# Kernel optimization log

Hardware: AMD Instinct MI355X
Metric: run time of the kernel (lower is better)

The kernel has to match this reference:

```python
import jax, jax.numpy as jnp
import numpy as np
import math

R, C, B, E, H, F = 64, 256, 1, 768, 12, 3072
D = E // H  # head dim = 64
EPS = 1e-6  # flax LayerNorm default


def _ln(x, s, b):
    mu = jnp.mean(x, axis=-1, keepdims=True)
    var = jnp.mean((x - mu) ** 2, axis=-1, keepdims=True)
    return (x - mu) * jax.lax.rsqrt(var + EPS) * s + b


def setup_inputs() -> dict:
    key = jax.random.key(0)
    ks = jax.random.split(key, 16)
    w = lambda k, sh: jax.random.normal(k, sh, jnp.float32) * 0.02
    z = lambda sh: jnp.zeros(sh, jnp.float32)
    return {
        "x": jax.random.normal(ks[0], (R, C, B, E), jnp.float32),
        "ln1_s": jnp.ones((E,), jnp.float32), "ln1_b": z((E,)),
        "r_wq": w(ks[1], (E, E)), "r_bq": z((E,)),
        "r_wk": w(ks[2], (E, E)), "r_bk": z((E,)),
        "r_wv": w(ks[3], (E, E)), "r_bv": z((E,)),
        "r_wo": w(ks[4], (E, E)), "r_bo": z((E,)),
        "ln2_s": jnp.ones((E,), jnp.float32), "ln2_b": z((E,)),
        "c_wq": w(ks[5], (E, E)), "c_bq": z((E,)),
        "c_wk": w(ks[6], (E, E)), "c_bk": z((E,)),
        "c_wv": w(ks[7], (E, E)), "c_bv": z((E,)),
        "c_wo": w(ks[8], (E, E)), "c_bo": z((E,)),
        "ln3_s": jnp.ones((E,), jnp.float32), "ln3_b": z((E,)),
        "f_w1": w(ks[9], (E, F)), "f_b1": z((F,)),
        "f_w2": w(ks[10], (F, E)), "f_b2": z((E,)),
    }


def reference(x, ln1_s, ln1_b, r_wq, r_bq, r_wk, r_bk, r_wv, r_bv, r_wo, r_bo,
              ln2_s, ln2_b, c_wq, c_bq, c_wk, c_bk, c_wv, c_bv, c_wo, c_bo,
              ln3_s, ln3_b, f_w1, f_b1, f_w2, f_b2):
    qkv = (R, C, B, H, D)
    # --- tied row self-attention (NOTE: original code has no residual adds) ---
    h = _ln(x, ln1_s, ln1_b)
    q = (h @ r_wq + r_bq).reshape(qkv) * (D ** -0.5 / math.sqrt(R))  # tied-row scaling
    k = (h @ r_wk + r_bk).reshape(qkv)
    v = (h @ r_wv + r_bv).reshape(qkv)
    aw = jnp.einsum('rinhd,rjnhd->hnij', q, k)  # single softmax tied across rows
    ap = jax.nn.softmax(aw, axis=-1)
    ctx = jnp.einsum('hnij,rjnhd->rinhd', ap, v).reshape(R, C, B, E)
    x = ctx @ r_wo + r_bo
    # --- column self-attention (per-column attention over rows) ---
    h = _ln(x, ln2_s, ln2_b)
    q = (h @ c_wq + c_bq).reshape(qkv) * (D ** -0.5)
    k = (h @ c_wk + c_bk).reshape(qkv)
    v = (h @ c_wv + c_bv).reshape(qkv)
    aw = jnp.einsum('icnhd,jcnhd->hcnij', q, k)
    ap = jax.nn.softmax(aw, axis=-1)
    ctx = jnp.einsum('hcnij,jcnhd->icnhd', ap, v).reshape(R, C, B, E)
    x = ctx @ c_wo + c_bo
    # --- FFN (gelu approximate=True matches flax default) ---
    h = _ln(x, ln3_s, ln3_b)
    return jax.nn.gelu(h @ f_w1 + f_b1) @ f_w2 + f_b2
```

## Files before the change

kernel.cpp:

```cpp
#include <hip/hip_runtime.h>
#include <hip/hip_bf16.h>
#include <stdint.h>
#include <stddef.h>

#define R_ 64
#define C_ 256
#define E_ 768
#define H_ 12
#define F_ 3072
#define D_ 64
#define NT_ (R_*C_)
#define HCRD_ ((size_t)H_*C_*R_*D_)

typedef float f32x4 __attribute__((ext_vector_type(4)));
typedef __bf16 bf16x8 __attribute__((ext_vector_type(8)));
typedef unsigned short us4 __attribute__((ext_vector_type(4)));
typedef unsigned short us8 __attribute__((ext_vector_type(8)));

typedef __attribute__((address_space(3))) uint32_t lds_u32;
typedef __attribute__((address_space(1))) uint32_t glb_u32;

__device__ __forceinline__ void gld16(const uint16_t* g, uint16_t* l) {
  __builtin_amdgcn_global_load_lds((const glb_u32*)g, (lds_u32*)l, 16, 0, 0);
}

__device__ __forceinline__ uint16_t f2b(float f) {
  __bf16 h = (__bf16)f;
  return *(uint16_t*)&h;
}

#define TILE_SYNC { asm volatile("s_waitcnt vmcnt(0)" ::: "memory"); \
                    __builtin_amdgcn_s_barrier(); \
                    __builtin_amdgcn_sched_barrier(0); }
#define BAR_ONLY  { __builtin_amdgcn_s_barrier(); __builtin_amdgcn_sched_barrier(0); }

enum { EP_F32B = 0, EP_GELU = 1, EP_AW = 2, EP_CTX = 3, EP_QKVROW = 4, EP_QKVCOL = 5 };

template<int EP, bool PERM>
__global__ __launch_bounds__(512, 2)
void gemm256(const uint16_t* __restrict__ A, const uint16_t* __restrict__ B,
             const float* __restrict__ bias, const float* __restrict__ biasK,
             const float* __restrict__ biasV, void* __restrict__ out,
             int N, int K, int lda, int ldb, float scale)
{
  __shared__ uint16_t As2[2][16384];
  __shared__ uint16_t Bs2[2][16384];
  const int tid  = threadIdx.x;
  const int wave = tid >> 6, lane = tid & 63;
  const int wm = wave >> 2, wn = wave & 3;
  const int lr = lane & 15, lq = lane >> 4;

  const int lin = blockIdx.x + gridDim.x * blockIdx.y;
  const int xcd = lin & 7, idx = lin >> 3;
  const int nbyx = gridDim.y >> 3;
  const int by = xcd * nbyx + idx / gridDim.x;
  const int bx = idx % gridDim.x;
  const long bm = (long)by * 256, bn = (long)bx * 256;

  const int r0 = tid >> 3;
  const int c8 = (((tid & 7) ^ (r0 & 7)) << 3);
  const uint16_t* aSrc[4];
  const uint16_t* bSrc[4];
#pragma unroll
  for (int i = 0; i < 4; ++i) {
    long am = bm + r0 + 64 * i;
    if constexpr (PERM) am = ((am & 63) << 8) | (am >> 6);
    aSrc[i] = A + am * (long)lda + c8;
    bSrc[i] = B + (bn + r0 + 64 * i) * (long)ldb + c8;
  }

  auto stage = [&](int u) {
    const int b = u & 1;
    const int kb = u << 6;
#pragma unroll
    for (int i = 0; i < 4; ++i) gld16(aSrc[i] + kb, &As2[b][tid * 8 + 4096 * i]);
#pragma unroll
    for (int i = 0; i < 4; ++i) gld16(bSrc[i] + kb, &Bs2[b][tid * 8 + 4096 * i]);
  };
  auto rdoff = [&](int row, int c) { return row * 64 + (((c ^ (row & 7))) << 3); };

  f32x4 acc[8][4];
#pragma unroll
  for (int i = 0; i < 8; ++i)
#pragma unroll
    for (int j = 0; j < 4; ++j) acc[i][j] = (f32x4){0.f, 0.f, 0.f, 0.f};

  const int nt = K >> 6;
  stage(0);
  TILE_SYNC;

  for (int t = 0; t < nt; ++t) {
    const int b = t & 1;
    if (t + 1 < nt) stage(t + 1);
#pragma unroll
    for (int kh = 0; kh < 2; ++kh) {
      const int c = kh * 4 + lq;
      bf16x8 bfr[4], afr[8];
#pragma unroll
      for (int i = 0; i < 4; ++i) bfr[i] = *(const bf16x8*)&Bs2[b][rdoff(wn * 64 + i * 16 + lr, c)];
#pragma unroll
      for (int i = 0; i < 8; ++i) afr[i] = *(const bf16x8*)&As2[b][rdoff(wm * 128 + i * 16 + lr, c)];
#pragma unroll
      for (int mi = 0; mi < 8; ++mi)
#pragma unroll
        for (int ni = 0; ni < 4; ++ni)
          acc[mi][ni] = __builtin_amdgcn_mfma_f32_16x16x32_bf16(afr[mi], bfr[ni], acc[mi][ni], 0, 0, 0);
    }
    if (t + 1 < nt) { TILE_SYNC; } else { BAR_ONLY; }
  }
  __syncthreads();

  if constexpr (EP == EP_F32B) {
#pragma unroll
    for (int mi = 0; mi < 8; ++mi)
#pragma unroll
      for (int ni = 0; ni < 4; ++ni)
#pragma unroll
        for (int r = 0; r < 4; ++r) {
          const long row = bm + wm * 128 + mi * 16 + lq * 4 + r;
          const long col = bn + wn * 64 + ni * 16 + lr;
          ((float*)out)[row * N + col] = acc[mi][ni][r] + bias[col];
        }
  } else {
    uint16_t* slabW = (wave < 4) ? &As2[0][wave * 8192] : &Bs2[0][(wave - 4) * 8192];
    const long colb = bn + wn * 64;
    int grp = 0; long cc0 = colb;
    const float* bb = bias;
    if constexpr (EP != EP_GELU) {
      grp = colb >= 1536 ? 2 : (colb >= 768 ? 1 : 0);
      cc0 = colb - (long)grp * 768;
      bb = grp == 0 ? bias : (grp == 1 ? biasK : biasV);
    }
    const bool tr = (EP != EP_GELU) && (grp == 2);
#pragma unroll
    for (int sub = 0; sub < 2; ++sub) {
      uint16_t* slab = slabW + sub * 4096;
      const long m0 = bm + wm * 128 + sub * 64;
#pragma unroll
      for (int mi = 0; mi < 4; ++mi)
#pragma unroll
        for (int ni = 0; ni < 4; ++ni)
#pragma unroll
          for (int r = 0; r < 4; ++r) {
            const int lrow = mi * 16 + lq * 4 + r;
            const int lcol = ni * 16 + lr;
            float val;
            if constexpr (EP == EP_GELU) {
              const float t = acc[sub * 4 + mi][ni][r] + bias[colb + lcol];
              const float u = 0.7978845608028654f * (t + 0.044715f * t * t * t);
              const float e = __expf(2.f * u);
              val = 0.5f * t * (2.f - 2.f / (e + 1.f));
            } else {
              val = acc[sub * 4 + mi][ni][r] + bb[cc0 + lcol];
              if (grp == 0) val *= scale;
            }
            const int sr = tr ? lcol : lrow;
            const int sc = tr ? lrow : lcol;
            const int psc = (sc & 7) | ((((sc >> 3) ^ (sr & 7))) << 3);
            slab[sr * 64 + psc] = f2b(val);
          }
      uint16_t* o16 = (uint16_t*)out;
      long obase, rstride;
      if constexpr (EP == EP_GELU) {
        obase = m0 * (long)N + colb; rstride = N;
      } else {
        const long h = cc0 >> 6;
        if constexpr (EP == EP_QKVROW) {
          const long rr = m0 >> 8, c0 = m0 & 255;
          if (grp < 2) { obase = (size_t)grp * HCRD_ + ((h * C_ + c0) * R_ + rr) * D_; rstride = R_ * D_; }
          else         { obase = 2 * HCRD_ + ((h * R_ + rr) * D_) * C_ + c0;           rstride = C_; }
        } else {
          const long cq = m0 >> 6;
          if (grp < 2) { obase = (size_t)grp * HCRD_ + ((h * C_ + cq) * R_) * D_; rstride = D_; }
          else         { obase = 2 * HCRD_ + ((h * C_ + cq) * D_) * R_;           rstride = R_; }
        }
      }
      const int rl = lane >> 3, chn = lane & 7;
#pragma unroll
      for (int pp = 0; pp < 8; ++pp) {
        const int srow = pp * 8 + rl;
        const int pch = chn ^ (srow & 7);
        us8 wv = *(const us8*)&slab[srow * 64 + pch * 8];
        *(us8*)(o16 + obase + (long)srow * rstride + chn * 8) = wv;
      }
    }
  }
}

template<int EP>
__global__ __launch_bounds__(256)
void gemm_bt(const uint16_t* __restrict__ A, const uint16_t* __restrict__ B,
             void* __restrict__ out,
             int M, int N, int K, int lda, int ldb, long sAz, long sBz)
{
  __shared__ uint16_t As[2][4096];
  __shared__ uint16_t Bs[2][4096];
  const int tid  = threadIdx.x;
  const int wave = tid >> 6, lane = tid & 63;
  const int z = blockIdx.z;

  const long bm = (long)blockIdx.y * 128;
  int kc = 0; long bnb = blockIdx.x;
  if constexpr (EP == EP_AW) { kc = blockIdx.x & 3; bnb = blockIdx.x >> 2; }
  const long bn = bnb * 128;
  const int wr = (wave >> 1) * 64;
  const int wc = (wave & 1) * 64;
  const int lr = lane & 15;
  const int lq = lane >> 4;

  const int t0 = tid, t1 = tid + 256;
  const int ar0 = t0 >> 2, ar1 = t1 >> 2;
  const int ac0 = (((t0 & 3) ^ ((ar0 >> 1) & 3)) * 8);
  const int ac1 = (((t1 & 3) ^ ((ar1 >> 1) & 3)) * 8);

  const uint16_t* a0p = A + (long)z * sAz + (bm + ar0) * (long)lda + (long)kc * 1024;
  const uint16_t* a1p = A + (long)z * sAz + (bm + ar1) * (long)lda + (long)kc * 1024;
  const uint16_t* b0p = B + (long)z * sBz + (bn + ar0) * (long)ldb + (long)kc * 1024;
  const uint16_t* b1p = B + (long)z * sBz + (bn + ar1) * (long)ldb + (long)kc * 1024;

  auto STAGE = [&](int bi, int kt) {
    gld16(a0p + kt + ac0, &As[bi][t0 * 8]);
    gld16(a1p + kt + ac1, &As[bi][t1 * 8]);
    gld16(b0p + kt + ac0, &Bs[bi][t0 * 8]);
    gld16(b1p + kt + ac1, &Bs[bi][t1 * 8]);
  };

  int apos[4], bpos[4];
#pragma unroll
  for (int i = 0; i < 4; ++i) {
    const int ra = wr + i * 16 + lr;
    const int rb = wc + i * 16 + lr;
    apos[i] = ra * 32 + (lq ^ ((ra >> 1) & 3)) * 8;
    bpos[i] = rb * 32 + (lq ^ ((rb >> 1) & 3)) * 8;
  }

  f32x4 acc[4][4];
#pragma unroll
  for (int i = 0; i < 4; ++i)
#pragma unroll
    for (int j = 0; j < 4; ++j) acc[i][j] = (f32x4){0.f, 0.f, 0.f, 0.f};

  const int nt = K >> 5;
  STAGE(0, 0);
  TILE_SYNC;

  for (int t = 0; t < nt; ++t) {
    const int b = t & 1;
    if (t + 1 < nt) STAGE(b ^ 1, (t + 1) << 5);
    bf16x8 af[4], bfm[4];
#pragma unroll
    for (int i = 0; i < 4; ++i) {
      af[i]  = *(const bf16x8*)&As[b][apos[i]];
      bfm[i] = *(const bf16x8*)&Bs[b][bpos[i]];
    }
#pragma unroll
    for (int mi = 0; mi < 4; ++mi)
#pragma unroll
      for (int ni = 0; ni < 4; ++ni)
        acc[mi][ni] = __builtin_amdgcn_mfma_f32_16x16x32_bf16(af[mi], bfm[ni], acc[mi][ni], 0, 0, 0);
    if (t + 1 < nt) { TILE_SYNC; }
  }

#pragma unroll
  for (int mi = 0; mi < 4; ++mi)
#pragma unroll
    for (int ni = 0; ni < 4; ++ni)
#pragma unroll
      for (int r = 0; r < 4; ++r) {
        const long row = bm + wr + mi * 16 + lq * 4 + r;
        const long col = bn + wc + ni * 16 + lr;
        if constexpr (EP == EP_AW) {
          ((float*)out)[((long)(z * 4 + kc) * M + row) * N + col] = acc[mi][ni][r];
        } else {
          ((uint16_t*)out)[((col >> 6) * C_ + row) * E_ + (long)z * 64 + (col & 63)] =
              f2b(acc[mi][ni][r]);
        }
      }
}

__global__ __launch_bounds__(256)
void ln_k(const float* __restrict__ x, const float* __restrict__ s, const float* __restrict__ b,
          uint16_t* __restrict__ out)
{
  const int wave = threadIdx.x >> 6, lane = threadIdx.x & 63;
  const long row = (long)blockIdx.x * 4 + wave;
  const float* xr = x + row * E_;
  f32x4 v[3];
  float sum = 0.f, sq = 0.f;
#pragma unroll
  for (int i = 0; i < 3; ++i) {
    v[i] = *(const f32x4*)(xr + (i * 64 + lane) * 4);
#pragma unroll
    for (int j = 0; j < 4; ++j) { sum += v[i][j]; sq += v[i][j] * v[i][j]; }
  }
#pragma unroll
  for (int m = 1; m < 64; m <<= 1) { sum += __shfl_xor(sum, m); sq += __shfl_xor(sq, m); }
  const float mu = sum * (1.f / E_);
  const float var = sq * (1.f / E_) - mu * mu;
  const float rs = rsqrtf(var + 1e-6f);
  uint16_t* orow = out + row * E_;
#pragma unroll
  for (int i = 0; i < 3; ++i) {
    const int e0 = (i * 64 + lane) * 4;
    us4 o;
#pragma unroll
    for (int j = 0; j < 4; ++j) o[j] = f2b((v[i][j] - mu) * rs * s[e0 + j] + b[e0 + j]);
    *(us4*)(orow + e0) = o;
  }
}

__global__ __launch_bounds__(256)
void softmax_k4(const float* __restrict__ aw4, uint16_t* __restrict__ ap)
{
  const int wave = threadIdx.x >> 6, lane = threadIdx.x & 63;
  const long row = (long)blockIdx.x * 4 + wave;
  const long h = row >> 8, i = row & 255;
  f32x4 v = (f32x4){0.f, 0.f, 0.f, 0.f};
#pragma unroll
  for (int kc = 0; kc < 4; ++kc) {
    f32x4 t = *(const f32x4*)(aw4 + (((h * 4 + kc) * C_ + i) * C_) + lane * 4);
#pragma unroll
    for (int j = 0; j < 4; ++j) v[j] += t[j];
  }
  float m = fmaxf(fmaxf(v[0], v[1]), fmaxf(v[2], v[3]));
#pragma unroll
  for (int k = 1; k < 64; k <<= 1) m = fmaxf(m, __shfl_xor(m, k));
  f32x4 e; float s = 0.f;
#pragma unroll
  for (int j = 0; j < 4; ++j) { e[j] = __expf(v[j] - m); s += e[j]; }
#pragma unroll
  for (int k = 1; k < 64; k <<= 1) s += __shfl_xor(s, k);
  const float inv = 1.f / s;
  us4 o;
#pragma unroll
  for (int j = 0; j < 4; ++j) o[j] = f2b(e[j] * inv);
  *(us4*)(ap + row * C_ + lane * 4) = o;
}

__global__ __launch_bounds__(256)
void tcvt(const float* __restrict__ in, uint16_t* __restrict__ out, int K, int N)
{
  __shared__ float t[32][33];
  const int tx = threadIdx.x, ty = threadIdx.y;
  const long k0 = (long)blockIdx.y * 32, n0 = (long)blockIdx.x * 32;
  for (int i = ty; i < 32; i += 8) t[i][tx] = in[(k0 + i) * N + n0 + tx];
  __syncthreads();
  for (int i = ty; i < 32; i += 8) out[(n0 + i) * K + k0 + tx] = f2b(t[tx][i]);
}

__global__ __launch_bounds__(256)
void tcvt8(const float* a0, const float* a1, const float* a2, const float* a3,
           const float* a4, const float* a5, const float* a6, const float* a7,
           uint16_t* o0, uint16_t* o1, uint16_t* o2, uint16_t* o3,
           uint16_t* o4, uint16_t* o5, uint16_t* o6, uint16_t* o7)
{
  __shared__ float t[32][33];
  const float* in; uint16_t* out;
  switch (blockIdx.z) {
    case 0: in = a0; out = o0; break;
    case 1: in = a1; out = o1; break;
    case 2: in = a2; out = o2; break;
    case 3: in = a3; out = o3; break;
    case 4: in = a4; out = o4; break;
    case 5: in = a5; out = o5; break;
    case 6: in = a6; out = o6; break;
    default: in = a7; out = o7; break;
  }
  const int tx = threadIdx.x, ty = threadIdx.y;
  const long k0 = (long)blockIdx.y * 32, n0 = (long)blockIdx.x * 32;
  for (int i = ty; i < 32; i += 8) t[i][tx] = in[(k0 + i) * E_ + n0 + tx];
  __syncthreads();
  for (int i = ty; i < 32; i += 8) out[(n0 + i) * E_ + k0 + tx] = f2b(t[tx][i]);
}

__global__ __launch_bounds__(64)
void colattn(const uint16_t* __restrict__ q, const uint16_t* __restrict__ k,
             const uint16_t* __restrict__ v, uint16_t* __restrict__ ctx)
{
  __shared__ uint16_t Qs[64 * 64];
  __shared__ uint16_t Ks[64 * 64];
  __shared__ uint16_t Vs[64 * 64];
  const int hc = blockIdx.x;
  const int h = hc >> 8, c = hc & 255;
  const int lane = threadIdx.x;
  const uint16_t* qb = q + (long)hc * (R_ * D_);
  const uint16_t* kb = k + (long)hc * (R_ * D_);
  const uint16_t* vb = v + (long)hc * (D_ * R_);
#pragma unroll
  for (int it = 0; it < 8; ++it) {
    const int o = (it * 64 + lane) * 8;
    gld16(qb + o, &Qs[o]);
    gld16(kb + o, &Ks[o]);
    gld16(vb + o, &Vs[o]);
  }
  asm volatile("s_waitcnt vmcnt(0)" ::: "memory");
  __builtin_amdgcn_sched_barrier(0);

  const int lr = lane & 15, lq = lane >> 4;
  f32x4 acc[4][4];
#pragma unroll
  for (int i = 0; i < 4; ++i)
#pragma unroll
    for (int j = 0; j < 4; ++j) acc[i][j] = (f32x4){0.f, 0.f, 0.f, 0.f};

#pragma unroll
  for (int kt = 0; kt < 2; ++kt) {
    bf16x8 af[4], bfm[4];
#pragma unroll
    for (int i = 0; i < 4; ++i) {
      af[i]  = *(const bf16x8*)&Qs[(i * 16 + lr) * 64 + kt * 32 + lq * 8];
      bfm[i] = *(const bf16x8*)&Ks[(i * 16 + lr) * 64 + kt * 32 + lq * 8];
    }
#pragma unroll
    for (int mi = 0; mi < 4; ++mi)
#pragma unroll
      for (int ni = 0; ni < 4; ++ni)
        acc[mi][ni] = __builtin_amdgcn_mfma_f32_16x16x32_bf16(af[mi], bfm[ni], acc[mi][ni], 0, 0, 0);
  }

#pragma unroll
  for (int mi = 0; mi < 4; ++mi) {
#pragma unroll
    for (int r = 0; r < 4; ++r) {
      float mx = fmaxf(fmaxf(acc[mi][0][r], acc[mi][1][r]), fmaxf(acc[mi][2][r], acc[mi][3][r]));
#pragma unroll
      for (int s = 1; s < 16; s <<= 1) mx = fmaxf(mx, __shfl_xor(mx, s));
      float e0 = __expf(acc[mi][0][r] - mx), e1 = __expf(acc[mi][1][r] - mx);
      float e2 = __expf(acc[mi][2][r] - mx), e3 = __expf(acc[mi][3][r] - mx);
      float sum = e0 + e1 + e2 + e3;
#pragma unroll
      for (int s = 1; s < 16; s <<= 1) sum += __shfl_xor(sum, s);
      const float inv = 1.f / sum;
      const int i = mi * 16 + lq * 4 + r;
      Qs[i * 64 +  0 + lr] = f2b(e0 * inv);
      Qs[i * 64 + 16 + lr] = f2b(e1 * inv);
      Qs[i * 64 + 32 + lr] = f2b(e2 * inv);
      Qs[i * 64 + 48 + lr] = f2b(e3 * inv);
    }
  }
  __syncthreads();

  f32x4 o_[4][4];
#pragma unroll
  for (int i = 0; i < 4; ++i)
#pragma unroll
    for (int j = 0; j < 4; ++j) o_[i][j] = (f32x4){0.f, 0.f, 0.f, 0.f};

#pragma unroll
  for (int kt = 0; kt < 2; ++kt) {
    bf16x8 pa[4], vv[4];
#pragma unroll
    for (int i = 0; i < 4; ++i) {
      pa[i] = *(const bf16x8*)&Qs[(i * 16 + lr) * 64 + kt * 32 + lq * 8];
      vv[i] = *(const bf16x8*)&Vs[(i * 16 + lr) * 64 + kt * 32 + lq * 8];
    }
#pragma unroll
    for (int mi = 0; mi < 4; ++mi)
#pragma unroll
      for (int ni = 0; ni < 4; ++ni)
        o_[mi][ni] = __builtin_amdgcn_mfma_f32_16x16x32_bf16(pa[mi], vv[ni], o_[mi][ni], 0, 0, 0);
  }

#pragma unroll
  for (int mi = 0; mi < 4; ++mi)
#pragma unroll
    for (int ni = 0; ni < 4; ++ni)
#pragma unroll
      for (int r = 0; r < 4; ++r) {
        const int i = mi * 16 + lq * 4 + r;
        const int d = ni * 16 + lr;
        ctx[((long)i * C_ + c) * E_ + h * 64 + d] = f2b(o_[mi][ni][r]);
      }
}

extern "C" void kernel_launch(void* const* d_in, const int* in_sizes, int n_in,
                              void* d_out, int out_size, void* d_ws, size_t ws_size,
                              hipStream_t stream)
{
  (void)in_sizes; (void)n_in; (void)out_size; (void)ws_size;
  const float* x     = (const float*)d_in[0];
  const float* ln1_s = (const float*)d_in[1];
  const float* ln1_b = (const float*)d_in[2];
  const float* r_wq  = (const float*)d_in[3];
  const float* r_bq  = (const float*)d_in[4];
  const float* r_wk  = (const float*)d_in[5];
  const float* r_bk  = (const float*)d_in[6];
  const float* r_wv  = (const float*)d_in[7];
  const float* r_bv  = (const float*)d_in[8];
  const float* r_wo  = (const float*)d_in[9];
  const float* r_bo  = (const float*)d_in[10];
  const float* ln2_s = (const float*)d_in[11];
  const float* ln2_b = (const float*)d_in[12];
  const float* c_wq  = (const float*)d_in[13];
  const float* c_bq  = (const float*)d_in[14];
  const float* c_wk  = (const float*)d_in[15];
  const float* c_bk  = (const float*)d_in[16];
  const float* c_wv  = (const float*)d_in[17];
  const float* c_bv  = (const float*)d_in[18];
  const float* c_wo  = (const float*)d_in[19];
  const float* c_bo  = (const float*)d_in[20];
  const float* ln3_s = (const float*)d_in[21];
  const float* ln3_b = (const float*)d_in[22];
  const float* f_w1  = (const float*)d_in[23];
  const float* f_b1  = (const float*)d_in[24];
  const float* f_w2  = (const float*)d_in[25];
  const float* f_b2  = (const float*)d_in[26];

  uint8_t* p = (uint8_t*)d_ws;
  auto take = [&p](size_t n) { uint8_t* r = p; p += (n + 255) & ~(size_t)255; return r; };

  uint16_t* wqkv1 = (uint16_t*)take((size_t)3 * E_ * E_ * 2);
  uint16_t* wqkv2 = (uint16_t*)take((size_t)3 * E_ * E_ * 2);
  uint16_t* rwoT  = (uint16_t*)take((size_t)E_ * E_ * 2);
  uint16_t* cwoT  = (uint16_t*)take((size_t)E_ * E_ * 2);
  uint16_t* w1T   = (uint16_t*)take((size_t)E_ * F_ * 2);
  uint16_t* w2T   = (uint16_t*)take((size_t)F_ * E_ * 2);
  uint16_t* hb    = (uint16_t*)take((size_t)NT_ * E_ * 2);
  uint16_t* qkvT  = (uint16_t*)take(3 * HCRD_ * 2);
  uint16_t* qT = qkvT, *kT = qkvT + HCRD_, *vT = qkvT + 2 * HCRD_;
  uint16_t* ctxb  = (uint16_t*)take((size_t)NT_ * E_ * 2);
  uint16_t* apb   = (uint16_t*)take((size_t)H_ * C_ * C_ * 2);
  uint16_t* g     = qkvT;
  float*    awb4  = (float*)ctxb;
  float*    x1    = (float*)d_out;

  const dim3 tb32(32, 8);
  tcvt8<<<dim3(E_ / 32, E_ / 32, 8), tb32, 0, stream>>>(
      r_wq, r_wk, r_wv, c_wq, c_wk, c_wv, r_wo, c_wo,
      wqkv1 + 0 * E_ * E_, wqkv1 + 1 * E_ * E_, wqkv1 + 2 * E_ * E_,
      wqkv2 + 0 * E_ * E_, wqkv2 + 1 * E_ * E_, wqkv2 + 2 * E_ * E_,
      rwoT, cwoT);
  tcvt<<<dim3(F_ / 32, E_ / 32), tb32, 0, stream>>>(f_w1, w1T, E_, F_);
  tcvt<<<dim3(E_ / 32, F_ / 32), tb32, 0, stream>>>(f_w2, w2T, F_, E_);

  ln_k<<<NT_ / 4, 256, 0, stream>>>(x, ln1_s, ln1_b, hb);
  gemm256<EP_QKVROW, false><<<dim3(9, 64), 512, 0, stream>>>(
      hb, wqkv1, r_bq, r_bk, r_bv, qkvT, 3 * E_, E_, E_, E_, 0.015625f);
  gemm_bt<EP_AW><<<dim3(8, 2, H_), 256, 0, stream>>>(
      qT, kT, awb4, C_, C_, 1024, R_ * D_, R_ * D_, (long)C_ * R_ * D_, (long)C_ * R_ * D_);
  softmax_k4<<<(H_ * C_) / 4, 256, 0, stream>>>(awb4, apb);
  gemm_bt<EP_CTX><<<dim3((R_ * D_) / 128, 2, H_), 256, 0, stream>>>(
      apb, vT, ctxb, C_, R_ * D_, C_, C_, C_, (long)C_ * C_, (long)R_ * D_ * C_);
  gemm256<EP_F32B, false><<<dim3(3, 64), 512, 0, stream>>>(
      ctxb, rwoT, r_bo, nullptr, nullptr, x1, E_, E_, E_, E_, 1.f);

  ln_k<<<NT_ / 4, 256, 0, stream>>>(x1, ln2_s, ln2_b, hb);
  gemm256<EP_QKVCOL, true><<<dim3(9, 64), 512, 0, stream>>>(
      hb, wqkv2, c_bq, c_bk, c_bv, qkvT, 3 * E_, E_, E_, E_, 0.125f);
  colattn<<<H_ * C_, 64, 0, stream>>>(qT, kT, vT, ctxb);
  gemm256<EP_F32B, false><<<dim3(3, 64), 512, 0, stream>>>(
      ctxb, cwoT, c_bo, nullptr, nullptr, x1, E_, E_, E_, E_, 1.f);

  ln_k<<<NT_ / 4, 256, 0, stream>>>(x1, ln3_s, ln3_b, hb);
  gemm256<EP_GELU, false><<<dim3(12, 64), 512, 0, stream>>>(
      hb, w1T, f_b1, nullptr, nullptr, g, F_, E_, E_, E_, 1.f);
  gemm256<EP_F32B, false><<<dim3(3, 64), 512, 0, stream>>>(
      g, w2T, f_b2, nullptr, nullptr, d_out, E_, F_, F_, F_, 1.f);
}
```

Measured before the change: 585.7 us.

## Split 256x256 GEMM K-tile into four half-stages with interleaved prefetch and priority

Restructures the main 256x256 GEMM mainloop so each 64-wide K tile is split into four LDS quarter-buffers (B/A for two 32-wide K halves). Global-to-LDS prefetch of the next tile is issued in four pieces, interleaved between MFMA phases, and partial vmcnt waits replace full drains. s_setprio raises wave priority around MFMA bursts. The block swizzle for XCD mapping is also simplified. This aims for finer-grained overlap of loads and compute, at the cost of more barriers per tile and tighter ordering assumptions on outstanding loads.

```diff
diff --git a/kernel.cpp b/kernel.cpp
--- a/kernel.cpp
+++ b/kernel.cpp
@@ -29,10 +29,9 @@
   return *(uint16_t*)&h;
 }
 
-#define TILE_SYNC { asm volatile("s_waitcnt vmcnt(0)" ::: "memory"); \
-                    __builtin_amdgcn_s_barrier(); \
-                    __builtin_amdgcn_sched_barrier(0); }
-#define BAR_ONLY  { __builtin_amdgcn_s_barrier(); __builtin_amdgcn_sched_barrier(0); }
+#define BAR      { asm volatile("s_barrier" ::: "memory"); }
+#define VMW4     { asm volatile("s_waitcnt vmcnt(4)" ::: "memory"); }
+#define VMW0     { asm volatile("s_waitcnt vmcnt(0)" ::: "memory"); }
 
 enum { EP_F32B = 0, EP_GELU = 1, EP_AW = 2, EP_CTX = 3, EP_QKVROW = 4, EP_QKVCOL = 5 };
 
@@ -43,41 +42,37 @@
              const float* __restrict__ biasV, void* __restrict__ out,
              int N, int K, int lda, int ldb, float scale)
 {
-  __shared__ uint16_t As2[2][16384];
-  __shared__ uint16_t Bs2[2][16384];
+  __shared__ uint16_t lds[2][4][8192];
   const int tid  = threadIdx.x;
   const int wave = tid >> 6, lane = tid & 63;
   const int wm = wave >> 2, wn = wave & 3;
   const int lr = lane & 15, lq = lane >> 4;
 
   const int lin = blockIdx.x + gridDim.x * blockIdx.y;
-  const int xcd = lin & 7, idx = lin >> 3;
-  const int nbyx = gridDim.y >> 3;
-  const int by = xcd * nbyx + idx / gridDim.x;
-  const int bx = idx % gridDim.x;
+  const int q8 = (gridDim.x * gridDim.y) >> 3;
+  const int wid = (lin & 7) * q8 + (lin >> 3);
+  const int bx = wid % gridDim.x, by = wid / gridDim.x;
   const long bm = (long)by * 256, bn = (long)bx * 256;
 
-  const int r0 = tid >> 3;
-  const int c8 = (((tid & 7) ^ (r0 & 7)) << 3);
-  const uint16_t* aSrc[4];
-  const uint16_t* bSrc[4];
-#pragma unroll
-  for (int i = 0; i < 4; ++i) {
-    long am = bm + r0 + 64 * i;
-    if constexpr (PERM) am = ((am & 63) << 8) | (am >> 6);
-    aSrc[i] = A + am * (long)lda + c8;
-    bSrc[i] = B + (bn + r0 + 64 * i) * (long)ldb + c8;
-  }
-
-  auto stage = [&](int u) {
-    const int b = u & 1;
-    const int kb = u << 6;
-#pragma unroll
-    for (int i = 0; i < 4; ++i) gld16(aSrc[i] + kb, &As2[b][tid * 8 + 4096 * i]);
-#pragma unroll
-    for (int i = 0; i < 4; ++i) gld16(bSrc[i] + kb, &Bs2[b][tid * 8 + 4096 * i]);
+  const int r0 = tid >> 2;
+  const int csw = (((tid & 3) ^ ((r0 >> 1) & 3)) * 8);
+  long am0 = bm + r0, am1 = bm + r0 + 128;
+  if constexpr (PERM) {
+    am0 = ((am0 & 63) << 8) | (am0 >> 6);
+    am1 = ((am1 & 63) << 8) | (am1 >> 6);
+  }
+  const uint16_t* aR0 = A + am0 * (long)lda + csw;
+  const uint16_t* aR1 = A + am1 * (long)lda + csw;
+  const uint16_t* bR0 = B + (bn + r0) * (long)ldb + csw;
+  const uint16_t* bR1 = B + (bn + r0 + 128) * (long)ldb + csw;
+
+  auto stageH = [&](int u, int j) {
+    const int kb = (u << 6) + ((j >> 1) << 5);
+    uint16_t* d = &lds[u & 1][j][0];
+    if (j & 1) { gld16(aR0 + kb, d + tid * 8); gld16(aR1 + kb, d + (tid + 512) * 8); }
+    else       { gld16(bR0 + kb, d + tid * 8); gld16(bR1 + kb, d + (tid + 512) * 8); }
   };
-  auto rdoff = [&](int row, int c) { return row * 64 + (((c ^ (row & 7))) << 3); };
+  auto off = [&](int row) { return row * 32 + ((lq ^ ((row >> 1) & 3)) * 8); };
 
   f32x4 acc[8][4];
 #pragma unroll
@@ -86,27 +81,80 @@
     for (int j = 0; j < 4; ++j) acc[i][j] = (f32x4){0.f, 0.f, 0.f, 0.f};
 
   const int nt = K >> 6;
-  stage(0);
-  TILE_SYNC;
+  stageH(0, 0); stageH(0, 1); stageH(0, 2); stageH(0, 3);
+  VMW4;
+  BAR;
 
   for (int t = 0; t < nt; ++t) {
     const int b = t & 1;
-    if (t + 1 < nt) stage(t + 1);
-#pragma unroll
-    for (int kh = 0; kh < 2; ++kh) {
-      const int c = kh * 4 + lq;
-      bf16x8 bfr[4], afr[8];
-#pragma unroll
-      for (int i = 0; i < 4; ++i) bfr[i] = *(const bf16x8*)&Bs2[b][rdoff(wn * 64 + i * 16 + lr, c)];
-#pragma unroll
-      for (int i = 0; i < 8; ++i) afr[i] = *(const bf16x8*)&As2[b][rdoff(wm * 128 + i * 16 + lr, c)];
-#pragma unroll
-      for (int mi = 0; mi < 8; ++mi)
-#pragma unroll
-        for (int ni = 0; ni < 4; ++ni)
-          acc[mi][ni] = __builtin_amdgcn_mfma_f32_16x16x32_bf16(afr[mi], bfr[ni], acc[mi][ni], 0, 0, 0);
-    }
-    if (t + 1 < nt) { TILE_SYNC; } else { BAR_ONLY; }
+    const uint16_t* Bk0 = &lds[b][0][0];
+    const uint16_t* Ak0 = &lds[b][1][0];
+    const uint16_t* Bk1 = &lds[b][2][0];
+    const uint16_t* Ak1 = &lds[b][3][0];
+    const bool pre = (t + 1 < nt);
+    bf16x8 bf[4], af[4];
+
+#pragma unroll
+    for (int i = 0; i < 4; ++i) {
+      bf[i] = *(const bf16x8*)&Bk0[off(wn * 64 + i * 16 + lr)];
+      af[i] = *(const bf16x8*)&Ak0[off(wm * 128 + i * 16 + lr)];
+    }
+    if (pre) stageH(t + 1, 0);
+    BAR;
+    __builtin_amdgcn_s_setprio(1);
+#pragma unroll
+    for (int mi = 0; mi < 4; ++mi)
+#pragma unroll
+      for (int ni = 0; ni < 4; ++ni)
+        acc[mi][ni] = __builtin_amdgcn_mfma_f32_16x16x32_bf16(af[mi], bf[ni], acc[mi][ni], 0, 0, 0);
+    __builtin_amdgcn_s_setprio(0);
+    BAR;
+
+#pragma unroll
+    for (int i = 0; i < 4; ++i)
+      af[i] = *(const bf16x8*)&Ak0[off(wm * 128 + 64 + i * 16 + lr)];
+    if (pre) stageH(t + 1, 1);
+    BAR;
+    __builtin_amdgcn_s_setprio(1);
+#pragma unroll
+    for (int mi = 0; mi < 4; ++mi)
+#pragma unroll
+      for (int ni = 0; ni < 4; ++ni)
+        acc[4 + mi][ni] = __builtin_amdgcn_mfma_f32_16x16x32_bf16(af[mi], bf[ni], acc[4 + mi][ni], 0, 0, 0);
+    __builtin_amdgcn_s_setprio(0);
+    if (pre) VMW4 else VMW0;
+    BAR;
+
+#pragma unroll
+    for (int i = 0; i < 4; ++i) {
+      bf[i] = *(const bf16x8*)&Bk1[off(wn * 64 + i * 16 + lr)];
+      af[i] = *(const bf16x8*)&Ak1[off(wm * 128 + i * 16 + lr)];
+    }
+    if (pre) stageH(t + 1, 2);
+    BAR;
+    __builtin_amdgcn_s_setprio(1);
+#pragma unroll
+    for (int mi = 0; mi < 4; ++mi)
+#pragma unroll
+      for (int ni = 0; ni < 4; ++ni)
+        acc[mi][ni] = __builtin_amdgcn_mfma_f32_16x16x32_bf16(af[mi], bf[ni], acc[mi][ni], 0, 0, 0);
+    __builtin_amdgcn_s_setprio(0);
+    BAR;
+
+#pragma unroll
+    for (int i = 0; i < 4; ++i)
+      af[i] = *(const bf16x8*)&Ak1[off(wm * 128 + 64 + i * 16 + lr)];
+    if (pre) stageH(t + 1, 3);
+    BAR;
+    __builtin_amdgcn_s_setprio(1);
+#pragma unroll
+    for (int mi = 0; mi < 4; ++mi)
+#pragma unroll
+      for (int ni = 0; ni < 4; ++ni)
+        acc[4 + mi][ni] = __builtin_amdgcn_mfma_f32_16x16x32_bf16(af[mi], bf[ni], acc[4 + mi][ni], 0, 0, 0);
+    __builtin_amdgcn_s_setprio(0);
+    if (pre) VMW4;
+    BAR;
   }
   __syncthreads();
 
@@ -122,7 +170,7 @@
           ((float*)out)[row * N + col] = acc[mi][ni][r] + bias[col];
         }
   } else {
-    uint16_t* slabW = (wave < 4) ? &As2[0][wave * 8192] : &Bs2[0][(wave - 4) * 8192];
+    uint16_t* slabW = ((uint16_t*)lds) + (size_t)wave * 8192;
     const long colb = bn + wn * 64;
     int grp = 0; long cc0 = colb;
     const float* bb = bias;
@@ -242,7 +290,7 @@
 
   const int nt = K >> 5;
   STAGE(0, 0);
-  TILE_SYNC;
+  VMW0; BAR;
 
   for (int t = 0; t < nt; ++t) {
     const int b = t & 1;
@@ -258,7 +306,7 @@
 #pragma unroll
       for (int ni = 0; ni < 4; ++ni)
         acc[mi][ni] = __builtin_amdgcn_mfma_f32_16x16x32_bf16(af[mi], bfm[ni], acc[mi][ni], 0, 0, 0);
-    if (t + 1 < nt) { TILE_SYNC; }
+    if (t + 1 < nt) { VMW0; BAR; }
   }
 
 #pragma unroll
```

New measurement: 552.7 us. 1.06x faster.

## Make gemm256 persistent over N tiles with cross-tile prefetch

Applied to the files above, without the earlier changes.

The 256x256 GEMM now takes a fixed grid of 4 column-slots per row block. Each block loops over a contiguous range of N tiles and prefetches the next tile's first K slab during the last K step of the current tile. This fits the QKV and FFN1 GEMMs into a single wave of 256 blocks, removing tail waves and overlapping epilogue with loads. The epilogue slab moves to the second LDS buffer so it does not clash with the in-flight prefetch into buffer 0. GELU also uses a fast reciprocal instead of a division. The risk is serialized per-block work, which reduces parallelism per row block.

```diff
diff --git a/kernel.cpp b/kernel.cpp
--- a/kernel.cpp
+++ b/kernel.cpp
@@ -29,10 +29,8 @@
   return *(uint16_t*)&h;
 }
 
-#define TILE_SYNC { asm volatile("s_waitcnt vmcnt(0)" ::: "memory"); \
-                    __builtin_amdgcn_s_barrier(); \
-                    __builtin_amdgcn_sched_barrier(0); }
-#define BAR_ONLY  { __builtin_amdgcn_s_barrier(); __builtin_amdgcn_sched_barrier(0); }
+#define BAR      { asm volatile("s_barrier" ::: "memory"); }
+#define VMW0     { asm volatile("s_waitcnt vmcnt(0)" ::: "memory"); }
 
 enum { EP_F32B = 0, EP_GELU = 1, EP_AW = 2, EP_CTX = 3, EP_QKVROW = 4, EP_QKVCOL = 5 };
 
@@ -51,137 +49,153 @@
   const int lr = lane & 15, lq = lane >> 4;
 
   const int lin = blockIdx.x + gridDim.x * blockIdx.y;
-  const int xcd = lin & 7, idx = lin >> 3;
-  const int nbyx = gridDim.y >> 3;
-  const int by = xcd * nbyx + idx / gridDim.x;
-  const int bx = idx % gridDim.x;
-  const long bm = (long)by * 256, bn = (long)bx * 256;
+  const int q8 = (gridDim.x * gridDim.y) >> 3;
+  const int wid = (lin & 7) * q8 + (lin >> 3);
+  const int px = wid % gridDim.x, by = wid / gridDim.x;
+  const long bm = (long)by * 256;
+
+  const int Nx = N >> 8, P = gridDim.x;
+  const int qq = Nx / P, rr = Nx - qq * P;
+  const int cnt   = qq + (px < rr ? 1 : 0);
+  const int start = px * qq + (px < rr ? px : rr);
 
   const int r0 = tid >> 3;
   const int c8 = (((tid & 7) ^ (r0 & 7)) << 3);
   const uint16_t* aSrc[4];
-  const uint16_t* bSrc[4];
+  long bRow[4];
 #pragma unroll
   for (int i = 0; i < 4; ++i) {
     long am = bm + r0 + 64 * i;
     if constexpr (PERM) am = ((am & 63) << 8) | (am >> 6);
     aSrc[i] = A + am * (long)lda + c8;
-    bSrc[i] = B + (bn + r0 + 64 * i) * (long)ldb + c8;
-  }
-
-  auto stage = [&](int u) {
-    const int b = u & 1;
-    const int kb = u << 6;
+    bRow[i] = (long)(r0 + 64 * i) * ldb;
+  }
+
+  auto stageA = [&](int u) {
+    const int b = u & 1, kb = u << 6;
 #pragma unroll
     for (int i = 0; i < 4; ++i) gld16(aSrc[i] + kb, &As2[b][tid * 8 + 4096 * i]);
-#pragma unroll
-    for (int i = 0; i < 4; ++i) gld16(bSrc[i] + kb, &Bs2[b][tid * 8 + 4096 * i]);
+  };
+  auto stageB = [&](int u, const uint16_t* bBase) {
+    const int b = u & 1, kb = u << 6;
+#pragma unroll
+    for (int i = 0; i < 4; ++i) gld16(bBase + bRow[i] + kb, &Bs2[b][tid * 8 + 4096 * i]);
   };
   auto rdoff = [&](int row, int c) { return row * 64 + (((c ^ (row & 7))) << 3); };
 
+  const int nt = K >> 6;
   f32x4 acc[8][4];
-#pragma unroll
-  for (int i = 0; i < 8; ++i)
-#pragma unroll
-    for (int j = 0; j < 4; ++j) acc[i][j] = (f32x4){0.f, 0.f, 0.f, 0.f};
-
-  const int nt = K >> 6;
-  stage(0);
-  TILE_SYNC;
-
-  for (int t = 0; t < nt; ++t) {
-    const int b = t & 1;
-    if (t + 1 < nt) stage(t + 1);
-#pragma unroll
-    for (int kh = 0; kh < 2; ++kh) {
-      const int c = kh * 4 + lq;
-      bf16x8 bfr[4], afr[8];
-#pragma unroll
-      for (int i = 0; i < 4; ++i) bfr[i] = *(const bf16x8*)&Bs2[b][rdoff(wn * 64 + i * 16 + lr, c)];
-#pragma unroll
-      for (int i = 0; i < 8; ++i) afr[i] = *(const bf16x8*)&As2[b][rdoff(wm * 128 + i * 16 + lr, c)];
+
+  { const uint16_t* b0 = B + c8 + ((long)start << 8) * ldb;
+    stageA(0); stageB(0, b0); }
+
+  for (int e = 0; e < cnt; ++e) {
+    const int bxi = start + e;
+    const long bn = (long)bxi << 8;
+    const uint16_t* bBase = B + c8 + bn * ldb;
+    const uint16_t* bNext = B + c8 + (bn + 256) * ldb;
+
+#pragma unroll
+    for (int i = 0; i < 8; ++i)
+#pragma unroll
+      for (int j = 0; j < 4; ++j) acc[i][j] = (f32x4){0.f, 0.f, 0.f, 0.f};
+
+    VMW0; BAR;
+
+    for (int t = 0; t < nt; ++t) {
+      const int b = t & 1;
+      if (t + 1 < nt)      { stageA(t + 1); stageB(t + 1, bBase); }
+      else if (e + 1 < cnt) { stageA(0);     stageB(0, bNext); }
+#pragma unroll
+      for (int kh = 0; kh < 2; ++kh) {
+        const int c = kh * 4 + lq;
+        bf16x8 bfr[4], afr[8];
+#pragma unroll
+        for (int i = 0; i < 4; ++i) bfr[i] = *(const bf16x8*)&Bs2[b][rdoff(wn * 64 + i * 16 + lr, c)];
+#pragma unroll
+        for (int i = 0; i < 8; ++i) afr[i] = *(const bf16x8*)&As2[b][rdoff(wm * 128 + i * 16 + lr, c)];
+#pragma unroll
+        for (int mi = 0; mi < 8; ++mi)
+#pragma unroll
+          for (int ni = 0; ni < 4; ++ni)
+            acc[mi][ni] = __builtin_amdgcn_mfma_f32_16x16x32_bf16(afr[mi], bfr[ni], acc[mi][ni], 0, 0, 0);
+      }
+      if (t + 1 < nt) { VMW0; BAR; }
+      else            { BAR; }
+    }
+
+    if constexpr (EP == EP_F32B) {
 #pragma unroll
       for (int mi = 0; mi < 8; ++mi)
 #pragma unroll
         for (int ni = 0; ni < 4; ++ni)
-          acc[mi][ni] = __builtin_amdgcn_mfma_f32_16x16x32_bf16(afr[mi], bfr[ni], acc[mi][ni], 0, 0, 0);
-    }
-    if (t + 1 < nt) { TILE_SYNC; } else { BAR_ONLY; }
-  }
-  __syncthreads();
-
-  if constexpr (EP == EP_F32B) {
-#pragma unroll
-    for (int mi = 0; mi < 8; ++mi)
-#pragma unroll
-      for (int ni = 0; ni < 4; ++ni)
-#pragma unroll
-        for (int r = 0; r < 4; ++r) {
-          const long row = bm + wm * 128 + mi * 16 + lq * 4 + r;
-          const long col = bn + wn * 64 + ni * 16 + lr;
-          ((float*)out)[row * N + col] = acc[mi][ni][r] + bias[col];
+#pragma unroll
+          for (int r = 0; r < 4; ++r) {
+            const long row = bm + wm * 128 + mi * 16 + lq * 4 + r;
+            const long col = bn + wn * 64 + ni * 16 + lr;
+            ((float*)out)[row * N + col] = acc[mi][ni][r] + bias[col];
+          }
+    } else {
+      uint16_t* slab = (wave < 4) ? &As2[1][wave * 4096] : &Bs2[1][(wave - 4) * 4096];
+      const long colb = bn + wn * 64;
+      int grp = 0; long cc0 = colb;
+      const float* bb = bias;
+      if constexpr (EP != EP_GELU) {
+        grp = colb >= 1536 ? 2 : (colb >= 768 ? 1 : 0);
+        cc0 = colb - (long)grp * 768;
+        bb = grp == 0 ? bias : (grp == 1 ? biasK : biasV);
+      }
+      const bool tr = (EP != EP_GELU) && (grp == 2);
+#pragma unroll
+      for (int sub = 0; sub < 2; ++sub) {
+        const long m0 = bm + wm * 128 + sub * 64;
+#pragma unroll
+        for (int mi = 0; mi < 4; ++mi)
+#pragma unroll
+          for (int ni = 0; ni < 4; ++ni)
+#pragma unroll
+            for (int r = 0; r < 4; ++r) {
+              const int lrow = mi * 16 + lq * 4 + r;
+              const int lcol = ni * 16 + lr;
+              float val;
+              if constexpr (EP == EP_GELU) {
+                const float t = acc[sub * 4 + mi][ni][r] + bias[colb + lcol];
+                const float u = 0.7978845608028654f * (t + 0.044715f * t * t * t);
+                const float e2 = __expf(2.f * u);
+                val = 0.5f * t * (2.f - 2.f * __builtin_amdgcn_rcpf(e2 + 1.f));
+              } else {
+                val = acc[sub * 4 + mi][ni][r] + bb[cc0 + lcol];
+                if (grp == 0) val *= scale;
+              }
+              const int sr = tr ? lcol : lrow;
+              const int sc = tr ? lrow : lcol;
+              const int psc = (sc & 7) | ((((sc >> 3) ^ (sr & 7))) << 3);
+              slab[sr * 64 + psc] = f2b(val);
+            }
+        uint16_t* o16 = (uint16_t*)out;
+        long obase, rstride;
+        if constexpr (EP == EP_GELU) {
+          obase = m0 * (long)N + colb; rstride = N;
+        } else {
+          const long h = cc0 >> 6;
+          if constexpr (EP == EP_QKVROW) {
+            const long rr2 = m0 >> 8, c0 = m0 & 255;
+            if (grp < 2) { obase = (size_t)grp * HCRD_ + ((h * C_ + c0) * R_ + rr2) * D_; rstride = R_ * D_; }
+            else         { obase = 2 * HCRD_ + ((h * R_ + rr2) * D_) * C_ + c0;           rstride = C_; }
+          } else {
+            const long cq = m0 >> 6;
+            if (grp < 2) { obase = (size_t)grp * HCRD_ + ((h * C_ + cq) * R_) * D_; rstride = D_; }
+            else         { obase = 2 * HCRD_ + ((h * C_ + cq) * D_) * R_;           rstride = R_; }
+          }
         }
-  } else {
-    uint16_t* slabW = (wave < 4) ? &As2[0][wave * 8192] : &Bs2[0][(wave - 4) * 8192];
-    const long colb = bn + wn * 64;
-    int grp = 0; long cc0 = colb;
-    const float* bb = bias;
-    if constexpr (EP != EP_GELU) {
-      grp = colb >= 1536 ? 2 : (colb >= 768 ? 1 : 0);
-      cc0 = colb - (long)grp * 768;
-      bb = grp == 0 ? bias : (grp == 1 ? biasK : biasV);
-    }
-    const bool tr = (EP != EP_GELU) && (grp == 2);
-#pragma unroll
-    for (int sub = 0; sub < 2; ++sub) {
-      uint16_t* slab = slabW + sub * 4096;
-      const long m0 = bm + wm * 128 + sub * 64;
-#pragma unroll
-      for (int mi = 0; mi < 4; ++mi)
-#pragma unroll
-        for (int ni = 0; ni < 4; ++ni)
-#pragma unroll
-          for (int r = 0; r < 4; ++r) {
-            const int lrow = mi * 16 + lq * 4 + r;
-            const int lcol = ni * 16 + lr;
-            float val;
-            if constexpr (EP == EP_GELU) {
-              const float t = acc[sub * 4 + mi][ni][r] + bias[colb + lcol];
-              const float u = 0.7978845608028654f * (t + 0.044715f * t * t * t);
-              const float e = __expf(2.f * u);
-              val = 0.5f * t * (2.f - 2.f / (e + 1.f));
-            } else {
-              val = acc[sub * 4 + mi][ni][r] + bb[cc0 + lcol];
-              if (grp == 0) val *= scale;
-            }
-            const int sr = tr ? lcol : lrow;
-            const int sc = tr ? lrow : lcol;
-            const int psc = (sc & 7) | ((((sc >> 3) ^ (sr & 7))) << 3);
-            slab[sr * 64 + psc] = f2b(val);
-          }
-      uint16_t* o16 = (uint16_t*)out;
-      long obase, rstride;
-      if constexpr (EP == EP_GELU) {
-        obase = m0 * (long)N + colb; rstride = N;
-      } else {
-        const long h = cc0 >> 6;
-        if constexpr (EP == EP_QKVROW) {
-          const long rr = m0 >> 8, c0 = m0 & 255;
-          if (grp < 2) { obase = (size_t)grp * HCRD_ + ((h * C_ + c0) * R_ + rr) * D_; rstride = R_ * D_; }
-          else         { obase = 2 * HCRD_ + ((h * R_ + rr) * D_) * C_ + c0;           rstride = C_; }
-        } else {
-          const long cq = m0 >> 6;
-          if (grp < 2) { obase = (size_t)grp * HCRD_ + ((h * C_ + cq) * R_) * D_; rstride = D_; }
-          else         { obase = 2 * HCRD_ + ((h * C_ + cq) * D_) * R_;           rstride = R_; }
+        const int rl = lane >> 3, chn = lane & 7;
+#pragma unroll
+        for (int pp = 0; pp < 8; ++pp) {
+          const int srow = pp * 8 + rl;
+          const int pch = chn ^ (srow & 7);
+          us8 wv = *(const us8*)&slab[srow * 64 + pch * 8];
+          *(us8*)(o16 + obase + (long)srow * rstride + chn * 8) = wv;
         }
-      }
-      const int rl = lane >> 3, chn = lane & 7;
-#pragma unroll
-      for (int pp = 0; pp < 8; ++pp) {
-        const int srow = pp * 8 + rl;
-        const int pch = chn ^ (srow & 7);
-        us8 wv = *(const us8*)&slab[srow * 64 + pch * 8];
-        *(us8*)(o16 + obase + (long)srow * rstride + chn * 8) = wv;
       }
     }
   }
@@ -242,7 +256,7 @@
 
   const int nt = K >> 5;
   STAGE(0, 0);
-  TILE_SYNC;
+  VMW0; BAR;
 
   for (int t = 0; t < nt; ++t) {
     const int b = t & 1;
@@ -258,7 +272,7 @@
 #pragma unroll
       for (int ni = 0; ni < 4; ++ni)
         acc[mi][ni] = __builtin_amdgcn_mfma_f32_16x16x32_bf16(af[mi], bfm[ni], acc[mi][ni], 0, 0, 0);
-    if (t + 1 < nt) { TILE_SYNC; }
+    if (t + 1 < nt) { VMW0; BAR; }
   }
 
 #pragma unroll
@@ -534,7 +548,7 @@
   tcvt<<<dim3(E_ / 32, F_ / 32), tb32, 0, stream>>>(f_w2, w2T, F_, E_);
 
   ln_k<<<NT_ / 4, 256, 0, stream>>>(x, ln1_s, ln1_b, hb);
-  gemm256<EP_QKVROW, false><<<dim3(9, 64), 512, 0, stream>>>(
+  gemm256<EP_QKVROW, false><<<dim3(4, 64), 512, 0, stream>>>(
       hb, wqkv1, r_bq, r_bk, r_bv, qkvT, 3 * E_, E_, E_, E_, 0.015625f);
   gemm_bt<EP_AW><<<dim3(8, 2, H_), 256, 0, stream>>>(
       qT, kT, awb4, C_, C_, 1024, R_ * D_, R_ * D_, (long)C_ * R_ * D_, (long)C_ * R_ * D_);
@@ -545,14 +559,14 @@
       ctxb, rwoT, r_bo, nullptr, nullptr, x1, E_, E_, E_, E_, 1.f);
 
   ln_k<<<NT_ / 4, 256, 0, stream>>>(x1, ln2_s, ln2_b, hb);
-  gemm256<EP_QKVCOL, true><<<dim3(9, 64), 512, 0, stream>>>(
+  gemm256<EP_QKVCOL, true><<<dim3(4, 64), 512, 0, stream>>>(
       hb, wqkv2, c_bq, c_bk, c_bv, qkvT, 3 * E_, E_, E_, E_, 0.125f);
   colattn<<<H_ * C_, 64, 0, stream>>>(qT, kT, vT, ctxb);
   gemm256<EP_F32B, false><<<dim3(3, 64), 512, 0, stream>>>(
       ctxb, cwoT, c_bo, nullptr, nullptr, x1, E_, E_, E_, E_, 1.f);
 
   ln_k<<<NT_ / 4, 256, 0, stream>>>(x1, ln3_s, ln3_b, hb);
-  gemm256<EP_GELU, false><<<dim3(12, 64), 512, 0, stream>>>(
+  gemm256<EP_GELU, false><<<dim3(4, 64), 512, 0, stream>>>(
       hb, w1T, f_b1, nullptr, nullptr, g, F_, E_, E_, E_, 1.f);
   gemm256<EP_F32B, false><<<dim3(3, 64), 512, 0, stream>>>(
       g, w2T, f_b2, nullptr, nullptr, d_out, E_, F_, F_, F_, 1.f);
```

After: 633.1 us. 8.1% more time.
